# Kernel optimization log

Measured on AMD Instinct MI355X. Metric: run time of the kernel, lower is better.

Reference implementation:

```python
import jax, jax.numpy as jnp
import numpy as np

NUM_LAYERS = 4
UNITS = 512
DX = 8e-6
WAVELENGTHS = np.array([4.5e-7, 5.32e-7, 6.33e-7], dtype=np.float32)
Z_LAYERS = 0.03
Z_PROP = 0.05
NUM_MODES = 16
BASE_IDX = 1  # base_wavelength_idx in source


def setup_inputs() -> dict:
    key = jax.random.key(0)
    k1, k2 = jax.random.split(key)
    C = len(WAVELENGTHS)
    x = jax.random.normal(k1, (NUM_MODES, C, UNITS, UNITS), dtype=jnp.float32)
    # phase = rand(units, units) * pi, one per layer
    phases = jax.random.uniform(k2, (NUM_LAYERS, UNITS, UNITS), dtype=jnp.float32) * np.pi
    # wavelength_coefficients initialized to base_wavelength / wl (learned params)
    base = WAVELENGTHS[BASE_IDX]
    coeffs = jnp.tile(jnp.asarray(base / WAVELENGTHS, dtype=jnp.float32), (NUM_LAYERS, 1))
    lams = jnp.asarray(WAVELENGTHS)
    return {"x": x, "phases": phases, "coeffs": coeffs, "lams": lams}


def _transfer_fn(lams, z, n, dx):
    # Band-limited angular-spectrum transfer function, per wavelength: [C, H, W]
    f = jnp.fft.fftfreq(n, d=dx).astype(jnp.float32)
    fx2 = f[None, :] ** 2 + f[:, None] ** 2          # [H, W]
    arg = (1.0 / lams)[:, None, None] ** 2 - fx2[None]  # [C, H, W]
    valid = arg > 0
    kz = 2.0 * jnp.pi * jnp.sqrt(jnp.where(valid, arg, 0.0))
    return jnp.where(valid, jnp.exp(1j * (kz * z).astype(jnp.float32)), 0.0)


def _propagate(field, Hf):
    # field: [B, C, H, W] complex; Hf: [C, H, W] — batched angular-spectrum step
    return jnp.fft.ifft2(jnp.fft.fft2(field) * Hf[None])


def reference(x, phases, coeffs, lams):
    n = x.shape[-1]
    H_layer = _transfer_fn(lams, Z_LAYERS, n, DX)  # inter-layer propagation
    H_final = _transfer_fn(lams, Z_PROP, n, DX)    # propagation to detector
    field = x.astype(jnp.complex64)
    for l in range(NUM_LAYERS):
        # per-wavelength effective phase: phase * coeff (depth_factor == 1)
        eff = phases[l][None, :, :] * coeffs[l][:, None, None]  # [C, H, W]
        field = field * jnp.exp(1j * eff)[None]
        field = _propagate(field, H_layer)
    field = _propagate(field, H_final)
    return jnp.abs(field) ** 2
```

## Files before the change

kernel.cpp:

```cpp
#include <hip/hip_runtime.h>
#include <hip/hip_fp16.h>
#include <math.h>


#define TWOPI_F 6.2831854820251465f
#define RSQ2    0.70710678f
#define NPIX    (48*512*512)

__device__ __forceinline__ float2 cadd(float2 a, float2 b){ return make_float2(a.x+b.x, a.y+b.y); }
__device__ __forceinline__ float2 csub(float2 a, float2 b){ return make_float2(a.x-b.x, a.y-b.y); }
__device__ __forceinline__ float2 cmul(float2 a, float2 b){ return make_float2(a.x*b.x - a.y*b.y, a.x*b.y + a.y*b.x); }

template<int S> __device__ __forceinline__ float2 mul_i(float2 a){
  return (S>0) ? make_float2(-a.y, a.x) : make_float2(a.y, -a.x);
}
template<int S> __device__ __forceinline__ float2 mul_w1(float2 a){
  return (S>0) ? make_float2(RSQ2*(a.x-a.y), RSQ2*(a.x+a.y))
               : make_float2(RSQ2*(a.x+a.y), RSQ2*(a.y-a.x));
}
template<int S> __device__ __forceinline__ float2 mul_w3(float2 a){
  return (S>0) ? make_float2(RSQ2*(-a.x-a.y), RSQ2*(a.x-a.y))
               : make_float2(RSQ2*(a.y-a.x), RSQ2*(-a.x-a.y));
}
template<int S> __device__ __forceinline__ float2 cmul_tw(float2 v, float2 w){
  float wy = (S>0) ? -w.y : w.y;
  return make_float2(v.x*w.x - v.y*wy, v.x*wy + v.y*w.x);
}

template<int S>
__device__ __forceinline__ void dft8(const float2* a, float2* d){
  float2 b0=cadd(a[0],a[4]), b1=cadd(a[1],a[5]), b2=cadd(a[2],a[6]), b3=cadd(a[3],a[7]);
  float2 b4=csub(a[0],a[4]);
  float2 b5=mul_w1<S>(csub(a[1],a[5]));
  float2 b6=mul_i<S> (csub(a[2],a[6]));
  float2 b7=mul_w3<S>(csub(a[3],a[7]));
  float2 c0=cadd(b0,b2), c2=csub(b0,b2);
  float2 c1=cadd(b1,b3), c3=mul_i<S>(csub(b1,b3));
  float2 c4=cadd(b4,b6), c6=csub(b4,b6);
  float2 c5=cadd(b5,b7), c7=mul_i<S>(csub(b5,b7));
  d[0]=cadd(c0,c1); d[1]=csub(c0,c1);
  d[2]=cadd(c2,c3); d[3]=csub(c2,c3);
  d[4]=cadd(c4,c5); d[5]=csub(c4,c5);
  d[6]=cadd(c6,c7); d[7]=csub(c6,c7);
}

__device__ __forceinline__ int SWZR(int i){ return i ^ ((i>>4)&7); }
__device__ __forceinline__ int CIDX(int e, int cx){
  return ((e ^ ((e>>3)&1))<<3) | (cx ^ ((e>>1)&7));
}

__device__ __forceinline__ void lds_fence(){ asm volatile("s_waitcnt lgkmcnt(0)" ::: "memory"); }

__device__ __forceinline__ void make_tw(int t, float2* tw0, float2* tw1){
  float sn, cs;
  __sincosf((TWOPI_F/512.0f)*(float)t, &sn, &cs);
  float2 w0 = make_float2(cs, -sn);
  tw0[0] = make_float2(1.0f, 0.0f);
  #pragma unroll
  for(int k=1;k<8;k++) tw0[k] = cmul(tw0[k-1], w0);
  int p = t>>3;
  __sincosf((TWOPI_F/64.0f)*(float)p, &sn, &cs);
  float2 w1 = make_float2(cs, -sn);
  tw1[0] = make_float2(1.0f, 0.0f);
  #pragma unroll
  for(int k=1;k<8;k++) tw1[k] = cmul(tw1[k-1], w1);
}

template<int S>
__device__ __forceinline__ void fft512_wv(float2* a, float2* o, float2* B, int t,
                                          float scale, const float2* tw0, const float2* tw1){
  const int km[8] = {0,4,2,6,1,5,3,7};
  float2 d[8];
  dft8<S>(a, d);
  #pragma unroll
  for(int k=0;k<8;k++)
    B[SWZR(8*t+k)] = (k==0) ? d[0] : cmul_tw<S>(d[km[k]], tw0[k]);
  lds_fence();
  #pragma unroll
  for(int r=0;r<8;r++) a[r] = B[SWZR(t+64*r)];
  lds_fence();
  dft8<S>(a, d);
  {
    int p = t>>3, q = t&7;
    #pragma unroll
    for(int k=0;k<8;k++)
      B[SWZR(q + 64*p + 8*k)] = (k==0) ? d[0] : cmul_tw<S>(d[km[k]], tw1[k]);
  }
  lds_fence();
  #pragma unroll
  for(int r=0;r<8;r++) a[r] = B[SWZR(t+64*r)];
  lds_fence();
  dft8<S>(a, d);
  #pragma unroll
  for(int k=0;k<8;k++) o[k] = make_float2(d[km[k]].x*scale, d[km[k]].y*scale);
}

template<int S>
__device__ __forceinline__ void fft512_cs(float2* a, float2* o, float2* B, int t, int cx,
                                          float scale, const float2* tw0, const float2* tw1){
  const int km[8] = {0,4,2,6,1,5,3,7};
  float2 d[8];
  dft8<S>(a, d);
  #pragma unroll
  for(int k=0;k<8;k++)
    B[CIDX(8*t+k, cx)] = (k==0) ? d[0] : cmul_tw<S>(d[km[k]], tw0[k]);
  __syncthreads();
  #pragma unroll
  for(int r=0;r<8;r++) a[r] = B[CIDX(t+64*r, cx)];
  __syncthreads();
  dft8<S>(a, d);
  {
    int p = t>>3, q = t&7;
    #pragma unroll
    for(int k=0;k<8;k++)
      B[CIDX(q + 64*p + 8*k, cx)] = (k==0) ? d[0] : cmul_tw<S>(d[km[k]], tw1[k]);
  }
  __syncthreads();
  #pragma unroll
  for(int r=0;r<8;r++) a[r] = B[CIDX(t+64*r, cx)];
  dft8<S>(a, d);
  #pragma unroll
  for(int k=0;k<8;k++) o[k] = make_float2(d[km[k]].x*scale, d[km[k]].y*scale);
}


struct AccH {
  __half2* p;
  __device__ __forceinline__ float2 ld(int i) const { return __half22float2(p[i]); }
  __device__ __forceinline__ void   st(int i, float2 v) const { p[i] = __floats2half2_rn(v.x, v.y); }
};
struct AccS {
  float* re; float* im;
  __device__ __forceinline__ float2 ld(int i) const { return make_float2(re[i], im[i]); }
  __device__ __forceinline__ void   st(int i, float2 v) const { re[i]=v.x; im[i]=v.y; }
};


__device__ __forceinline__ float2 phase_of(float kz, float zf){
  float tt = __fmul_rn(kz, zf);
  double dt = (double)tt;
  double q  = rint(dt * 0.15915494309189535);
  double rr = fma(-q, 6.283185307179586, dt);
  float sn, cs; __sincosf((float)rr, &sn, &cs);
  return make_float2(cs, sn);
}

__global__ __launch_bounds__(256) void k_htab(const float* __restrict__ lams,
                                              float2* __restrict__ H1, float2* __restrict__ H12){
  int e = blockIdx.x*256 + threadIdx.x;
  int c = e >> 18, fy = (e>>9)&511, col = e&511;
  const float lam = lams[c];
  const float il  = 1.0f / lam;
  const float il2 = __fmul_rn(il, il);
  const float DEN = (float)(512.0 * 8e-6);
  int   sx  = (col < 256) ? col : col - 512;
  int   sy  = (fy  < 256) ? fy  : fy  - 512;
  float fxv = (float)sx / DEN, fyv = (float)sy / DEN;
  float arg = __fsub_rn(il2, __fadd_rn(__fmul_rn(fxv,fxv), __fmul_rn(fyv,fyv)));
  float2 h1 = make_float2(0.0f,0.0f), h12 = h1;
  if(arg > 0.0f){
    float s  = (float)sqrt((double)arg);
    float kz = __fmul_rn(6.2831854820251465f, s);
    h1  = phase_of(kz, 0.03f);
    h12 = cmul(h1, phase_of(kz, 0.05f));
  }
  H1[e] = h1; H12[e] = h12;
}


template<class Acc>
__global__ __launch_bounds__(256) void k_row_first(
    const float* __restrict__ x, Acc f,
    const float* __restrict__ phases, const float* __restrict__ coeffs)
{
  __shared__ float2 lds[4][512];
  const int w = threadIdx.x >> 6, t = threadIdx.x & 63;
  const int img = blockIdx.x, c = img % 3;
  const int row = (blockIdx.y<<2) + w;
  const int base = (img*512 + row)*512;
  const float* ph = phases + row*512;
  const float coeff = coeffs[c];
  float2 tw0[8], tw1[8]; make_tw(t, tw0, tw1);
  float2 a[8], o[8];
  #pragma unroll
  for(int r=0;r<8;r++){
    int i = t + (r<<6);
    float xv = x[base+i];
    float th = __fmul_rn(ph[i], coeff);
    float sn, cs; __sincosf(th, &sn, &cs);
    a[r] = make_float2(xv*cs, xv*sn);
  }
  fft512_wv<-1>(a, o, lds[w], t, 1.0f, tw0, tw1);
  #pragma unroll
  for(int k=0;k<8;k++){ int i=t+(k<<6); f.st(base+i, o[k]); }
}

template<class Acc>
__global__ __launch_bounds__(256) void k_row_mid(
    Acc f, const float* __restrict__ phases, const float* __restrict__ coeffs, int layer)
{
  __shared__ float2 lds[4][512];
  const int w = threadIdx.x >> 6, t = threadIdx.x & 63;
  const int img = blockIdx.x, c = img % 3;
  const int row = (blockIdx.y<<2) + w;
  const int base = (img*512 + row)*512;
  const float* ph = phases + (layer*512 + row)*512;
  const float coeff = coeffs[layer*3 + c];
  float2 tw0[8], tw1[8]; make_tw(t, tw0, tw1);
  float2 a[8], o[8], pv[8];
  #pragma unroll
  for(int r=0;r<8;r++){
    int i=t+(r<<6); a[r]=f.ld(base+i);
    float th = __fmul_rn(ph[i], coeff);
    float sn, cs; __sincosf(th, &sn, &cs);
    pv[r] = make_float2(cs, sn);
  }
  fft512_wv<+1>(a, o, lds[w], t, 1.0f/512.0f, tw0, tw1);
  #pragma unroll
  for(int k=0;k<8;k++) a[k] = cmul(o[k], pv[k]);
  fft512_wv<-1>(a, o, lds[w], t, 1.0f, tw0, tw1);
  #pragma unroll
  for(int k=0;k<8;k++){ int i=t+(k<<6); f.st(base+i, o[k]); }
}

template<class Acc>
__global__ __launch_bounds__(256) void k_row_last(
    Acc f, float* __restrict__ out)
{
  __shared__ float2 lds[4][512];
  const int w = threadIdx.x >> 6, t = threadIdx.x & 63;
  const int img = blockIdx.x;
  const int row = (blockIdx.y<<2) + w;
  const int base = (img*512 + row)*512;
  float2 tw0[8], tw1[8]; make_tw(t, tw0, tw1);
  float2 a[8], o[8];
  #pragma unroll
  for(int r=0;r<8;r++){ int i=t+(r<<6); a[r]=f.ld(base+i); }
  fft512_wv<+1>(a, o, lds[w], t, 1.0f/512.0f, tw0, tw1);
  #pragma unroll
  for(int k=0;k<8;k++){ int i=t+(k<<6); out[base+i] = o[k].x*o[k].x + o[k].y*o[k].y; }
}


template<class Acc, bool TAB>
__global__ __launch_bounds__(512, 4) void k_col8(
    Acc f, const float2* __restrict__ Htab, const float* __restrict__ lams, float z1, float z2)
{
  __shared__ float2 lds[512*8];
  const int cx = threadIdx.x & 7, t = threadIdx.x >> 3;
  const int img = blockIdx.x, c = img % 3;
  const int col = (blockIdx.y<<3) + cx;
  const int ibase = (img<<18) + col;
  float2 tw0[8], tw1[8]; make_tw(t, tw0, tw1);
  float2 a[8], o[8], h[8];
  #pragma unroll
  for(int r=0;r<8;r++){ int gi = ibase + ((t+(r<<6))<<9); a[r]=f.ld(gi); }
  if(TAB){
    const float2* Hrow = Htab + (c<<18) + col;
    #pragma unroll
    for(int k=0;k<8;k++) h[k] = Hrow[(t+(k<<6))<<9];
  } else {
    const float lam = lams[c];
    const float il  = 1.0f / lam;
    const float il2 = __fmul_rn(il, il);
    const float DEN = (float)(512.0 * 8e-6);
    int   sx  = (col < 256) ? col : col - 512;
    float fxv = (float)sx / DEN;
    float fx2 = __fmul_rn(fxv, fxv);
    #pragma unroll
    for(int k=0;k<8;k++){
      int fy = t + (k<<6);
      int sy = (fy < 256) ? fy : fy - 512;
      float fyv = (float)sy / DEN;
      float arg = __fsub_rn(il2, __fadd_rn(fx2, __fmul_rn(fyv,fyv)));
      h[k] = make_float2(0.0f, 0.0f);
      if(arg > 0.0f){
        float s  = (float)sqrt((double)arg);
        float kz = __fmul_rn(6.2831854820251465f, s);
        h[k] = phase_of(kz, z1);
        if(z2 != 0.0f) h[k] = cmul(h[k], phase_of(kz, z2));
      }
    }
  }
  fft512_cs<-1>(a, o, lds, t, cx, 1.0f, tw0, tw1);
  #pragma unroll
  for(int k=0;k<8;k++) a[k] = cmul(o[k], h[k]);
  __syncthreads();
  fft512_cs<+1>(a, o, lds, t, cx, 1.0f/512.0f, tw0, tw1);
  #pragma unroll
  for(int k=0;k<8;k++){ int gi = ibase + ((t+(k<<6))<<9); f.st(gi, o[k]); }
}


extern "C" void kernel_launch(void* const* d_in, const int* in_sizes, int n_in,
                              void* d_out, int out_size, void* d_ws, size_t ws_size,
                              hipStream_t stream)
{
  const float* x      = (const float*)d_in[0];
  const float* phases = (const float*)d_in[1];
  const float* coeffs = (const float*)d_in[2];
  const float* lams   = (const float*)d_in[3];
  float* out = (float*)d_out;

  const size_t fldH = (size_t)NPIX*4;
  const size_t splB = (size_t)NPIX*4;
  const size_t tabB = (size_t)3*512*512*8;

  dim3 gA(48,128), bA(256);
  dim3 gB(48,64),  bB(512);
  dim3 gH(3*512*512/256), bH(256);

  if(ws_size >= fldH + 2*tabB){
    AccH f { (__half2*)d_ws };
    float2* H1  = (float2*)((char*)d_ws + fldH);
    float2* H12 = H1 + 3*512*512;
    k_htab<<<gH, bH, 0, stream>>>(lams, H1, H12);
    k_row_first<AccH><<<gA, bA, 0, stream>>>(x, f, phases, coeffs);
    for(int l=1; l<=3; l++){
      k_col8<AccH,true><<<gB, bB, 0, stream>>>(f, H1, lams, 0.03f, 0.0f);
      k_row_mid<AccH><<<gA, bA, 0, stream>>>(f, phases, coeffs, l);
    }
    k_col8<AccH,true><<<gB, bB, 0, stream>>>(f, H12, lams, 0.03f, 0.0f);
    k_row_last<AccH><<<gA, bA, 0, stream>>>(f, out);
  } else if(ws_size >= splB + 2*tabB){
    AccS f { out, (float*)d_ws };
    float2* H1  = (float2*)((char*)d_ws + splB);
    float2* H12 = H1 + 3*512*512;
    k_htab<<<gH, bH, 0, stream>>>(lams, H1, H12);
    k_row_first<AccS><<<gA, bA, 0, stream>>>(x, f, phases, coeffs);
    for(int l=1; l<=3; l++){
      k_col8<AccS,true><<<gB, bB, 0, stream>>>(f, H1, lams, 0.03f, 0.0f);
      k_row_mid<AccS><<<gA, bA, 0, stream>>>(f, phases, coeffs, l);
    }
    k_col8<AccS,true><<<gB, bB, 0, stream>>>(f, H12, lams, 0.03f, 0.0f);
    k_row_last<AccS><<<gA, bA, 0, stream>>>(f, out);
  } else {
    AccS f { out, (float*)d_ws };
    k_row_first<AccS><<<gA, bA, 0, stream>>>(x, f, phases, coeffs);
    for(int l=1; l<=3; l++){
      k_col8<AccS,false><<<gB, bB, 0, stream>>>(f, nullptr, lams, 0.03f, 0.0f);
      k_row_mid<AccS><<<gA, bA, 0, stream>>>(f, phases, coeffs, l);
    }
    k_col8<AccS,false><<<gB, bB, 0, stream>>>(f, nullptr, lams, 0.03f, 0.05f);
    k_row_last<AccS><<<gA, bA, 0, stream>>>(f, out);
  }
}
```

Baseline: 292.5 us.

## Stage 16-column fp16 tiles in LDS for coalesced column FFT passes

Adds a column-FFT kernel that loads a 512x16 tile of half2 field values into shared memory with row-contiguous, coalesced 64-byte segments. Each wavefront then runs the forward FFT, multiplies by the transfer function and runs the inverse FFT on two columns from the tile, writing results back before one coalesced store. This replaces the strided 8-column access of the old column kernel in the fp16 workspace path. It uses more LDS per block (tile plus per-wave scratch), which lowers occupancy, and serialises the two columns per wave.

```diff
diff --git a/kernel.cpp b/kernel.cpp
--- a/kernel.cpp
+++ b/kernel.cpp
@@ -45,6 +45,9 @@
 }
 
 __device__ __forceinline__ int SWZR(int i){ return i ^ ((i>>4)&7); }
+__device__ __forceinline__ int TIDX(int row, int cc){
+  return (row<<4) | ((cc + row + (row>>4)) & 15);
+}
 __device__ __forceinline__ int CIDX(int e, int cx){
   return ((e ^ ((e>>3)&1))<<3) | (cx ^ ((e>>1)&7));
 }
@@ -242,6 +245,64 @@
 }
 
 
+__global__ __launch_bounds__(512, 3) void k_colw(
+    __half2* __restrict__ F, const float2* __restrict__ Htab)
+{
+  __shared__ unsigned int tile[512*16];
+  __shared__ float2 priv[8][512];
+  const int tid = threadIdx.x;
+  const int w = tid >> 6, t = tid & 63;
+  const int cx = tid & 15, t2 = tid >> 4;
+  const int img = blockIdx.x, c = img % 3;
+  const int col0 = blockIdx.y << 4;
+  const int gbase = (img<<18) + col0;
+
+  #pragma unroll
+  for(int r=0;r<16;r++){
+    int row = t2 + (r<<5);
+    unsigned int v = *reinterpret_cast<const unsigned int*>(F + gbase + (row<<9) + cx);
+    tile[TIDX(row, cx)] = v;
+  }
+  __syncthreads();
+
+  float2 tw0[8], tw1[8]; make_tw(t, tw0, tw1);
+
+  #pragma unroll 1
+  for(int cc=0; cc<2; cc++){
+    const int C = (w<<1) + cc;
+    float2 a[8], o[8], h[8];
+    #pragma unroll
+    for(int r=0;r<8;r++){
+      int row = t + (r<<6);
+      unsigned int v = tile[TIDX(row, C)];
+      __half2 hv; *reinterpret_cast<unsigned int*>(&hv) = v;
+      a[r] = __half22float2(hv);
+    }
+    const float2* Hcol = Htab + (c<<18) + col0 + C;
+    #pragma unroll
+    for(int k=0;k<8;k++) h[k] = Hcol[(t+(k<<6))<<9];
+    fft512_wv<-1>(a, o, priv[w], t, 1.0f, tw0, tw1);
+    #pragma unroll
+    for(int k=0;k<8;k++) a[k] = cmul(o[k], h[k]);
+    fft512_wv<+1>(a, o, priv[w], t, 1.0f/512.0f, tw0, tw1);
+    #pragma unroll
+    for(int k=0;k<8;k++){
+      int row = t + (k<<6);
+      __half2 hv = __floats2half2_rn(o[k].x, o[k].y);
+      tile[TIDX(row, C)] = *reinterpret_cast<unsigned int*>(&hv);
+    }
+  }
+  __syncthreads();
+
+  #pragma unroll
+  for(int r=0;r<16;r++){
+    int row = t2 + (r<<5);
+    unsigned int v = tile[TIDX(row, cx)];
+    *reinterpret_cast<unsigned int*>(F + gbase + (row<<9) + cx) = v;
+  }
+}
+
+
 template<class Acc, bool TAB>
 __global__ __launch_bounds__(512, 4) void k_col8(
     Acc f, const float2* __restrict__ Htab, const float* __restrict__ lams, float z1, float z2)
@@ -307,6 +368,7 @@
   const size_t tabB = (size_t)3*512*512*8;
 
   dim3 gA(48,128), bA(256);
+  dim3 gW(48,32),  bW(512);
   dim3 gB(48,64),  bB(512);
   dim3 gH(3*512*512/256), bH(256);
 
@@ -317,10 +379,10 @@
     k_htab<<<gH, bH, 0, stream>>>(lams, H1, H12);
     k_row_first<AccH><<<gA, bA, 0, stream>>>(x, f, phases, coeffs);
     for(int l=1; l<=3; l++){
-      k_col8<AccH,true><<<gB, bB, 0, stream>>>(f, H1, lams, 0.03f, 0.0f);
+      k_colw<<<gW, bW, 0, stream>>>((__half2*)d_ws, H1);
       k_row_mid<AccH><<<gA, bA, 0, stream>>>(f, phases, coeffs, l);
     }
-    k_col8<AccH,true><<<gB, bB, 0, stream>>>(f, H12, lams, 0.03f, 0.0f);
+    k_colw<<<gW, bW, 0, stream>>>((__half2*)d_ws, H12);
     k_row_last<AccH><<<gA, bA, 0, stream>>>(f, out);
   } else if(ws_size >= splB + 2*tabB){
     AccS f { out, (float*)d_ws };
```

After: 459.3 us. 57.0% more time.

## Replace strided column FFT passes with transpose-based row FFTs using ping-pong buffers

Applied to the files above, without the earlier changes.

The fast path now keeps the half-precision field transposed between passes. Each kernel does contiguous row FFTs for 16 rows per block, stages the results in an LDS tile, and writes them out transposed with 16-element runs instead of doing strided column FFTs. Two half2 buffers are ping-ponged between k_prop (column FFT, multiply by H, inverse) and k_mid (row FFT, phase mask, forward). This removes the large-stride column accesses, but the fast path now needs twice the workspace for the field, and the transposed writes are only partly coalesced.

```diff
diff --git a/kernel.cpp b/kernel.cpp
--- a/kernel.cpp
+++ b/kernel.cpp
@@ -45,8 +45,15 @@
 }
 
 __device__ __forceinline__ int SWZR(int i){ return i ^ ((i>>4)&7); }
-__device__ __forceinline__ int CIDX(int e, int cx){
-  return ((e ^ ((e>>3)&1))<<3) | (cx ^ ((e>>1)&7));
+__device__ __forceinline__ int TI(int p, int j){ return (p<<4) | ((j + p) & 15); }
+
+__device__ __forceinline__ unsigned int pkh(float2 v){
+  __half2 h = __floats2half2_rn(v.x, v.y);
+  return *reinterpret_cast<unsigned int*>(&h);
+}
+__device__ __forceinline__ float2 upkh(unsigned int u){
+  __half2 h; *reinterpret_cast<unsigned int*>(&h) = u;
+  return __half22float2(h);
 }
 
 __device__ __forceinline__ void lds_fence(){ asm volatile("s_waitcnt lgkmcnt(0)" ::: "memory"); }
@@ -90,34 +97,6 @@
   #pragma unroll
   for(int r=0;r<8;r++) a[r] = B[SWZR(t+64*r)];
   lds_fence();
-  dft8<S>(a, d);
-  #pragma unroll
-  for(int k=0;k<8;k++) o[k] = make_float2(d[km[k]].x*scale, d[km[k]].y*scale);
-}
-
-template<int S>
-__device__ __forceinline__ void fft512_cs(float2* a, float2* o, float2* B, int t, int cx,
-                                          float scale, const float2* tw0, const float2* tw1){
-  const int km[8] = {0,4,2,6,1,5,3,7};
-  float2 d[8];
-  dft8<S>(a, d);
-  #pragma unroll
-  for(int k=0;k<8;k++)
-    B[CIDX(8*t+k, cx)] = (k==0) ? d[0] : cmul_tw<S>(d[km[k]], tw0[k]);
-  __syncthreads();
-  #pragma unroll
-  for(int r=0;r<8;r++) a[r] = B[CIDX(t+64*r, cx)];
-  __syncthreads();
-  dft8<S>(a, d);
-  {
-    int p = t>>3, q = t&7;
-    #pragma unroll
-    for(int k=0;k<8;k++)
-      B[CIDX(q + 64*p + 8*k, cx)] = (k==0) ? d[0] : cmul_tw<S>(d[km[k]], tw1[k]);
-  }
-  __syncthreads();
-  #pragma unroll
-  for(int r=0;r<8;r++) a[r] = B[CIDX(t+64*r, cx)];
   dft8<S>(a, d);
   #pragma unroll
   for(int k=0;k<8;k++) o[k] = make_float2(d[km[k]].x*scale, d[km[k]].y*scale);
@@ -168,6 +147,145 @@
 }
 
 
+__global__ __launch_bounds__(512, 2) void k_first(
+    const float* __restrict__ x, __half2* __restrict__ FT,
+    const float* __restrict__ phases, const float* __restrict__ coeffs)
+{
+  __shared__ float2 priv[8][512];
+  __shared__ unsigned int tile[512*16];
+  const int w = threadIdx.x >> 6, t = threadIdx.x & 63;
+  const int img = blockIdx.x, c = img % 3;
+  const int r0 = blockIdx.y << 4;
+  const float coeff = coeffs[c];
+  float2 tw0[8], tw1[8]; make_tw(t, tw0, tw1);
+  #pragma unroll 1
+  for(int cc=0; cc<2; cc++){
+    const int j = (w<<1)|cc, row = r0 + j;
+    const int base = (img*512 + row)*512;
+    const float* ph = phases + row*512;
+    float2 a[8], o[8];
+    #pragma unroll
+    for(int r=0;r<8;r++){
+      int i = t + (r<<6);
+      float xv = x[base+i];
+      float th = __fmul_rn(ph[i], coeff);
+      float sn, cs; __sincosf(th, &sn, &cs);
+      a[r] = make_float2(xv*cs, xv*sn);
+    }
+    fft512_wv<-1>(a, o, priv[w], t, 1.0f, tw0, tw1);
+    #pragma unroll
+    for(int k=0;k<8;k++) tile[TI(t+(k<<6), j)] = pkh(o[k]);
+  }
+  __syncthreads();
+  const int cx = threadIdx.x & 15, cr = threadIdx.x >> 4;
+  __half2* dst = FT + (img<<18) + r0 + cx;
+  #pragma unroll
+  for(int g=0; g<16; g++){
+    int p = cr + (g<<5);
+    *reinterpret_cast<unsigned int*>(dst + (p<<9)) = tile[TI(p, cx)];
+  }
+}
+
+__global__ __launch_bounds__(512, 2) void k_prop(
+    const __half2* __restrict__ FT, __half2* __restrict__ FN,
+    const float2* __restrict__ Htab)
+{
+  __shared__ float2 priv[8][512];
+  __shared__ unsigned int tile[512*16];
+  const int w = threadIdx.x >> 6, t = threadIdx.x & 63;
+  const int img = blockIdx.x, c = img % 3;
+  const int f0 = blockIdx.y << 4;
+  float2 tw0[8], tw1[8]; make_tw(t, tw0, tw1);
+  #pragma unroll 1
+  for(int cc=0; cc<2; cc++){
+    const int j = (w<<1)|cc, fx = f0 + j;
+    const __half2* src  = FT + (img<<18) + (fx<<9);
+    const float2*  Hrow = Htab + (c<<18) + (fx<<9);
+    float2 a[8], o[8];
+    #pragma unroll
+    for(int r=0;r<8;r++)
+      a[r] = upkh(*reinterpret_cast<const unsigned int*>(src + t + (r<<6)));
+    fft512_wv<-1>(a, o, priv[w], t, 1.0f, tw0, tw1);
+    #pragma unroll
+    for(int k=0;k<8;k++){
+      float2 h = Hrow[t + (k<<6)];
+      a[k] = cmul(o[k], h);
+    }
+    fft512_wv<+1>(a, o, priv[w], t, 1.0f/512.0f, tw0, tw1);
+    #pragma unroll
+    for(int k=0;k<8;k++) tile[TI(t+(k<<6), j)] = pkh(o[k]);
+  }
+  __syncthreads();
+  const int cx = threadIdx.x & 15, cr = threadIdx.x >> 4;
+  __half2* dst = FN + (img<<18) + f0 + cx;
+  #pragma unroll
+  for(int g=0; g<16; g++){
+    int p = cr + (g<<5);
+    *reinterpret_cast<unsigned int*>(dst + (p<<9)) = tile[TI(p, cx)];
+  }
+}
+
+__global__ __launch_bounds__(512, 2) void k_mid(
+    const __half2* __restrict__ FN, __half2* __restrict__ FT,
+    const float* __restrict__ phases, const float* __restrict__ coeffs, int layer)
+{
+  __shared__ float2 priv[8][512];
+  __shared__ unsigned int tile[512*16];
+  const int w = threadIdx.x >> 6, t = threadIdx.x & 63;
+  const int img = blockIdx.x, c = img % 3;
+  const int r0 = blockIdx.y << 4;
+  const float coeff = coeffs[layer*3 + c];
+  float2 tw0[8], tw1[8]; make_tw(t, tw0, tw1);
+  #pragma unroll 1
+  for(int cc=0; cc<2; cc++){
+    const int j = (w<<1)|cc, row = r0 + j;
+    const __half2* src = FN + (img<<18) + (row<<9);
+    const float* ph = phases + (layer*512 + row)*512;
+    float2 a[8], o[8];
+    #pragma unroll
+    for(int r=0;r<8;r++)
+      a[r] = upkh(*reinterpret_cast<const unsigned int*>(src + t + (r<<6)));
+    fft512_wv<+1>(a, o, priv[w], t, 1.0f/512.0f, tw0, tw1);
+    #pragma unroll
+    for(int k=0;k<8;k++){
+      int i = t + (k<<6);
+      float th = __fmul_rn(ph[i], coeff);
+      float sn, cs; __sincosf(th, &sn, &cs);
+      a[k] = cmul(o[k], make_float2(cs, sn));
+    }
+    fft512_wv<-1>(a, o, priv[w], t, 1.0f, tw0, tw1);
+    #pragma unroll
+    for(int k=0;k<8;k++) tile[TI(t+(k<<6), j)] = pkh(o[k]);
+  }
+  __syncthreads();
+  const int cx = threadIdx.x & 15, cr = threadIdx.x >> 4;
+  __half2* dst = FT + (img<<18) + r0 + cx;
+  #pragma unroll
+  for(int g=0; g<16; g++){
+    int p = cr + (g<<5);
+    *reinterpret_cast<unsigned int*>(dst + (p<<9)) = tile[TI(p, cx)];
+  }
+}
+
+template<class Acc>
+__global__ __launch_bounds__(256) void k_row_last(
+    Acc f, float* __restrict__ out)
+{
+  __shared__ float2 lds[4][512];
+  const int w = threadIdx.x >> 6, t = threadIdx.x & 63;
+  const int img = blockIdx.x;
+  const int row = (blockIdx.y<<2) + w;
+  const int base = (img*512 + row)*512;
+  float2 tw0[8], tw1[8]; make_tw(t, tw0, tw1);
+  float2 a[8], o[8];
+  #pragma unroll
+  for(int r=0;r<8;r++){ int i=t+(r<<6); a[r]=f.ld(base+i); }
+  fft512_wv<+1>(a, o, lds[w], t, 1.0f/512.0f, tw0, tw1);
+  #pragma unroll
+  for(int k=0;k<8;k++){ int i=t+(k<<6); out[base+i] = o[k].x*o[k].x + o[k].y*o[k].y; }
+}
+
+
 template<class Acc>
 __global__ __launch_bounds__(256) void k_row_first(
     const float* __restrict__ x, Acc f,
@@ -223,24 +341,37 @@
   for(int k=0;k<8;k++){ int i=t+(k<<6); f.st(base+i, o[k]); }
 }
 
-template<class Acc>
-__global__ __launch_bounds__(256) void k_row_last(
-    Acc f, float* __restrict__ out)
-{
-  __shared__ float2 lds[4][512];
-  const int w = threadIdx.x >> 6, t = threadIdx.x & 63;
-  const int img = blockIdx.x;
-  const int row = (blockIdx.y<<2) + w;
-  const int base = (img*512 + row)*512;
-  float2 tw0[8], tw1[8]; make_tw(t, tw0, tw1);
-  float2 a[8], o[8];
-  #pragma unroll
-  for(int r=0;r<8;r++){ int i=t+(r<<6); a[r]=f.ld(base+i); }
-  fft512_wv<+1>(a, o, lds[w], t, 1.0f/512.0f, tw0, tw1);
-  #pragma unroll
-  for(int k=0;k<8;k++){ int i=t+(k<<6); out[base+i] = o[k].x*o[k].x + o[k].y*o[k].y; }
-}
-
+__device__ __forceinline__ int CIDX(int e, int cx){
+  return ((e ^ ((e>>3)&1))<<3) | (cx ^ ((e>>1)&7));
+}
+
+template<int S>
+__device__ __forceinline__ void fft512_cs(float2* a, float2* o, float2* B, int t, int cx,
+                                          float scale, const float2* tw0, const float2* tw1){
+  const int km[8] = {0,4,2,6,1,5,3,7};
+  float2 d[8];
+  dft8<S>(a, d);
+  #pragma unroll
+  for(int k=0;k<8;k++)
+    B[CIDX(8*t+k, cx)] = (k==0) ? d[0] : cmul_tw<S>(d[km[k]], tw0[k]);
+  __syncthreads();
+  #pragma unroll
+  for(int r=0;r<8;r++) a[r] = B[CIDX(t+64*r, cx)];
+  __syncthreads();
+  dft8<S>(a, d);
+  {
+    int p = t>>3, q = t&7;
+    #pragma unroll
+    for(int k=0;k<8;k++)
+      B[CIDX(q + 64*p + 8*k, cx)] = (k==0) ? d[0] : cmul_tw<S>(d[km[k]], tw1[k]);
+  }
+  __syncthreads();
+  #pragma unroll
+  for(int r=0;r<8;r++) a[r] = B[CIDX(t+64*r, cx)];
+  dft8<S>(a, d);
+  #pragma unroll
+  for(int k=0;k<8;k++) o[k] = make_float2(d[km[k]].x*scale, d[km[k]].y*scale);
+}
 
 template<class Acc, bool TAB>
 __global__ __launch_bounds__(512, 4) void k_col8(
@@ -306,42 +437,45 @@
   const size_t splB = (size_t)NPIX*4;
   const size_t tabB = (size_t)3*512*512*8;
 
-  dim3 gA(48,128), bA(256);
-  dim3 gB(48,64),  bB(512);
+  dim3 gT(48,32),  bT(512);
+  dim3 gL(48,128), bL(256);
   dim3 gH(3*512*512/256), bH(256);
 
-  if(ws_size >= fldH + 2*tabB){
-    AccH f { (__half2*)d_ws };
-    float2* H1  = (float2*)((char*)d_ws + fldH);
+  if(ws_size >= 2*fldH + 2*tabB){
+    __half2* fldA = (__half2*)d_ws;
+    __half2* fldB = (__half2*)((char*)d_ws + fldH);
+    float2* H1  = (float2*)((char*)d_ws + 2*fldH);
     float2* H12 = H1 + 3*512*512;
     k_htab<<<gH, bH, 0, stream>>>(lams, H1, H12);
-    k_row_first<AccH><<<gA, bA, 0, stream>>>(x, f, phases, coeffs);
+    k_first<<<gT, bT, 0, stream>>>(x, fldA, phases, coeffs);
     for(int l=1; l<=3; l++){
-      k_col8<AccH,true><<<gB, bB, 0, stream>>>(f, H1, lams, 0.03f, 0.0f);
-      k_row_mid<AccH><<<gA, bA, 0, stream>>>(f, phases, coeffs, l);
-    }
-    k_col8<AccH,true><<<gB, bB, 0, stream>>>(f, H12, lams, 0.03f, 0.0f);
-    k_row_last<AccH><<<gA, bA, 0, stream>>>(f, out);
+      k_prop<<<gT, bT, 0, stream>>>(fldA, fldB, H1);
+      k_mid <<<gT, bT, 0, stream>>>(fldB, fldA, phases, coeffs, l);
+    }
+    k_prop<<<gT, bT, 0, stream>>>(fldA, fldB, H12);
+    k_row_last<AccH><<<gL, bL, 0, stream>>>(AccH{fldB}, out);
   } else if(ws_size >= splB + 2*tabB){
     AccS f { out, (float*)d_ws };
     float2* H1  = (float2*)((char*)d_ws + splB);
     float2* H12 = H1 + 3*512*512;
     k_htab<<<gH, bH, 0, stream>>>(lams, H1, H12);
-    k_row_first<AccS><<<gA, bA, 0, stream>>>(x, f, phases, coeffs);
+    dim3 gB(48,64), bB(512);
+    k_row_first<AccS><<<gL, bL, 0, stream>>>(x, f, phases, coeffs);
     for(int l=1; l<=3; l++){
       k_col8<AccS,true><<<gB, bB, 0, stream>>>(f, H1, lams, 0.03f, 0.0f);
-      k_row_mid<AccS><<<gA, bA, 0, stream>>>(f, phases, coeffs, l);
+      k_row_mid<AccS><<<gL, bL, 0, stream>>>(f, phases, coeffs, l);
     }
     k_col8<AccS,true><<<gB, bB, 0, stream>>>(f, H12, lams, 0.03f, 0.0f);
-    k_row_last<AccS><<<gA, bA, 0, stream>>>(f, out);
+    k_row_last<AccS><<<gL, bL, 0, stream>>>(f, out);
   } else {
     AccS f { out, (float*)d_ws };
-    k_row_first<AccS><<<gA, bA, 0, stream>>>(x, f, phases, coeffs);
+    dim3 gB(48,64), bB(512);
+    k_row_first<AccS><<<gL, bL, 0, stream>>>(x, f, phases, coeffs);
     for(int l=1; l<=3; l++){
       k_col8<AccS,false><<<gB, bB, 0, stream>>>(f, nullptr, lams, 0.03f, 0.0f);
-      k_row_mid<AccS><<<gA, bA, 0, stream>>>(f, phases, coeffs, l);
+      k_row_mid<AccS><<<gL, bL, 0, stream>>>(f, phases, coeffs, l);
     }
     k_col8<AccS,false><<<gB, bB, 0, stream>>>(f, nullptr, lams, 0.03f, 0.05f);
-    k_row_last<AccS><<<gA, bA, 0, stream>>>(f, out);
-  }
-}
+    k_row_last<AccS><<<gL, bL, 0, stream>>>(f, out);
+  }
+}
```

Result: no change. 291.4 us (-0.4%).
